# Performance work log

Measured on AMD Instinct MI355X. Metric: run time of the kernel, lower is better.

Reference implementation:

```python
import jax, jax.numpy as jnp
import numpy as np

N = 12000
F_IN = 256
F_OUT = 256


def setup_inputs() -> dict:
    key = jax.random.key(0)
    k1, k2, k3, k4, k5, k6 = jax.random.split(key, 6)
    stdv = 1.0 / np.sqrt(F_OUT)
    inp = {
        "input": jax.random.normal(k1, (N, F_IN), dtype=jnp.float32),
        "adj": jax.random.uniform(k2, (N, N), dtype=jnp.float32),
        "incidence_matrix": jax.random.uniform(k3, (N, N), dtype=jnp.float32),
        "weight": jax.random.uniform(k4, (F_IN, F_OUT), jnp.float32, -stdv, stdv),
        "attn": jax.random.uniform(k5, (F_IN, 1), jnp.float32, -stdv, stdv),
        "alpha": jax.random.uniform(k6, (1,), dtype=jnp.float32),
    }
    return inp


def reference(input, adj, incidence_matrix, weight, attn, alpha):
    # support1 = softmax over nodes of per-node attention score: [N, 1]
    scores = input @ attn                      # [N, 1]
    support1 = jax.nn.softmax(scores, axis=0)  # [N, 1]
    # diag(support1) @ input is just a per-row scale (avoid NxN diag)
    scaled = support1 * input                  # [N, F_in]
    support3 = adj @ scaled                    # [N, F_in]
    support4 = support3 + alpha * input        # [N, F_in]
    support = support4 @ weight                # [N, F_out]
    output = incidence_matrix @ support        # [N, F_out]
    return output
```

## Files before the change

kernel.cpp:

```cpp
#include <hip/hip_runtime.h>
#include <hip/hip_bf16.h>

typedef __bf16 bf16_t;
typedef __bf16 bf16x8v __attribute__((ext_vector_type(8)));
typedef __bf16 bf16x4v __attribute__((ext_vector_type(4)));
typedef float f32x4 __attribute__((ext_vector_type(4)));

#define NN 12000
#define FF 256

__global__ void scores_kernel(const float* __restrict__ input, const float* __restrict__ attn,
                              float* __restrict__ scores)
{
    int tid  = threadIdx.x;
    int lane = tid & 63;
    int r    = blockIdx.x * 4 + (tid >> 6);
    const float4 x = *(const float4*)(input + (size_t)r * FF + lane * 4);
    const float4 a = *(const float4*)(attn + lane * 4);
    float s = x.x * a.x + x.y * a.y + x.z * a.z + x.w * a.w;
#pragma unroll
    for (int off = 32; off > 0; off >>= 1) s += __shfl_down(s, off);
    if (lane == 0) scores[r] = s;
}

__global__ void softmax_kernel(float* __restrict__ s, int n)
{
    __shared__ float red[16];
    __shared__ float bc[2];
    int tid = threadIdx.x, lane = tid & 63, w = tid >> 6;

    float mx = -1e30f;
    for (int i = tid; i < n; i += 1024) mx = fmaxf(mx, s[i]);
#pragma unroll
    for (int o = 32; o > 0; o >>= 1) mx = fmaxf(mx, __shfl_down(mx, o));
    if (lane == 0) red[w] = mx;
    __syncthreads();
    if (tid == 0) {
        float m = red[0];
        for (int i = 1; i < 16; ++i) m = fmaxf(m, red[i]);
        bc[0] = m;
    }
    __syncthreads();
    float M = bc[0];

    float sum = 0.f;
    for (int i = tid; i < n; i += 1024) sum += __expf(s[i] - M);
#pragma unroll
    for (int o = 32; o > 0; o >>= 1) sum += __shfl_down(sum, o);
    if (lane == 0) red[w] = sum;
    __syncthreads();
    if (tid == 0) {
        float t = 0.f;
        for (int i = 0; i < 16; ++i) t += red[i];
        bc[1] = t;
    }
    __syncthreads();
    float inv = 1.0f / bc[1];
    for (int i = tid; i < n; i += 1024) s[i] = __expf(s[i] - M) * inv;
}

__global__ void transpose_scale_kernel(const float* __restrict__ src, const float* __restrict__ p,
                                       bf16_t* __restrict__ dst, int R)
{
    __shared__ float T[64][65];
    int tid = threadIdx.x;
    int r0 = blockIdx.x * 64;
    int c0 = blockIdx.y * 64;
    int j = (tid & 15) * 4;
#pragma unroll
    for (int i = 0; i < 4; ++i) {
        int rl = (tid >> 4) + 16 * i;
        int gr = r0 + rl;
        float4 v = {0.f, 0.f, 0.f, 0.f};
        float sc = 1.f;
        if (gr < R) {
            v = *(const float4*)(src + (size_t)gr * FF + c0 + j);
            if (p) sc = p[gr];
        }
        T[rl][j + 0] = v.x * sc;
        T[rl][j + 1] = v.y * sc;
        T[rl][j + 2] = v.z * sc;
        T[rl][j + 3] = v.w * sc;
    }
    __syncthreads();
#pragma unroll
    for (int i = 0; i < 2; ++i) {
        int idx = tid + 256 * i;
        int cl = idx >> 3;
        int rr = (idx & 7) * 8;
        if (r0 + rr < R) {
            bf16x8v v;
#pragma unroll
            for (int e = 0; e < 8; ++e) v[e] = (bf16_t)T[rr + e][cl];
            *(bf16x8v*)(dst + (size_t)(c0 + cl) * R + r0 + rr) = v;
        }
    }
}

template <int MODE>
__global__ __launch_bounds__(256, 3)
void gemm_kernel(const float* __restrict__ A, const bf16_t* __restrict__ Bt,
                 float* __restrict__ Cpart, size_t part_stride,
                 bf16_t* __restrict__ Ct,
                 int M, int K, int sps, int total_steps)
{
    constexpr int LDSA  = 64 * 40;
    constexpr int LDSB  = 256 * 40;
    constexpr int STAGE = LDSA + LDSB;
    constexpr int EPI   = 256 * 72;
    __shared__ __align__(16) bf16_t smem[(MODE == 1) ? (STAGE > EPI ? STAGE : EPI) : STAGE];
    bf16_t* As = smem;
    bf16_t* Bs = smem + LDSA;

    const int tid  = threadIdx.x;
    const int wave = tid >> 6;
    const int lane = tid & 63;
    const int quad = lane >> 4;
    const int l16  = lane & 15;
    const int row0   = blockIdx.x * 64;
    const int step0  = blockIdx.y * sps;
    const int nsteps = min(sps, total_steps - step0);

    f32x4 acc[4][4];
#pragma unroll
    for (int i = 0; i < 4; ++i)
#pragma unroll
        for (int j = 0; j < 4; ++j)
            acc[i][j] = (f32x4){0.f, 0.f, 0.f, 0.f};

    const int a_kq = (tid & 7) * 4;
    const int a_r  = tid >> 3;
    const int b_kq = (tid & 3) * 8;
    const int b_n  = tid >> 2;
    const int qk   = quad * 8;

    for (int s = 0; s < nsteps; ++s) {
        const int k0 = (step0 + s) * 32;
#pragma unroll
        for (int i = 0; i < 2; ++i) {
            int r = a_r + 32 * i;
            int gr = row0 + r;
            float4 v = {0.f, 0.f, 0.f, 0.f};
            if (gr < M) v = *(const float4*)(A + (size_t)gr * K + k0 + a_kq);
            bf16x4v w;
            w[0] = (bf16_t)v.x; w[1] = (bf16_t)v.y; w[2] = (bf16_t)v.z; w[3] = (bf16_t)v.w;
            *(bf16x4v*)(As + r * 40 + a_kq) = w;
        }
#pragma unroll
        for (int i = 0; i < 4; ++i) {
            int n = b_n + 64 * i;
            bf16x8v v = *(const bf16x8v*)(Bt + (size_t)n * K + k0 + b_kq);
            *(bf16x8v*)(Bs + n * 40 + b_kq) = v;
        }
        __syncthreads();
        bf16x8v af[4], bfr[4];
#pragma unroll
        for (int t = 0; t < 4; ++t) {
            af[t]  = *(const bf16x8v*)(As + (16 * t + l16) * 40 + qk);
            bfr[t] = *(const bf16x8v*)(Bs + (wave * 64 + 16 * t + l16) * 40 + qk);
        }
#pragma unroll
        for (int im = 0; im < 4; ++im)
#pragma unroll
            for (int in = 0; in < 4; ++in)
                acc[im][in] = __builtin_amdgcn_mfma_f32_16x16x32_bf16(af[im], bfr[in], acc[im][in], 0, 0, 0);
        __syncthreads();
    }

    if (MODE == 0) {
        float* Cp = Cpart + (size_t)blockIdx.y * part_stride;
#pragma unroll
        for (int im = 0; im < 4; ++im)
#pragma unroll
            for (int in = 0; in < 4; ++in) {
                int n = wave * 64 + 16 * in + l16;
#pragma unroll
                for (int rg = 0; rg < 4; ++rg) {
                    int r = row0 + 16 * im + 4 * quad + rg;
                    if (r < M) Cp[(size_t)r * FF + n] = acc[im][in][rg];
                }
            }
    } else {
        constexpr int TS = 72;
        bf16_t* T = smem;
#pragma unroll
        for (int im = 0; im < 4; ++im)
#pragma unroll
            for (int in = 0; in < 4; ++in) {
                int n  = wave * 64 + 16 * in + l16;
                int mb = 16 * im + 4 * quad;
                bf16x4v w;
#pragma unroll
                for (int rg = 0; rg < 4; ++rg) w[rg] = (bf16_t)acc[im][in][rg];
                *(bf16x4v*)(T + n * TS + mb) = w;
            }
        __syncthreads();
#pragma unroll
        for (int i = 0; i < 8; ++i) {
            int idx = tid + 256 * i;
            int n  = idx >> 3;
            int mc = (idx & 7) * 8;
            if (row0 + mc < M) {
                bf16x8v v = *(const bf16x8v*)(T + n * TS + mc);
                *(bf16x8v*)(Ct + (size_t)n * M + row0 + mc) = v;
            }
        }
    }
}

__global__ void reduce_parts_kernel(const float* __restrict__ parts, size_t part_stride,
                                    int nsplit,
                                    const float* __restrict__ addsrc, const float* __restrict__ alpha,
                                    float* __restrict__ out, int count4)
{
    int i = blockIdx.x * 256 + threadIdx.x;
    if (i >= count4) return;
    f32x4 s = ((const f32x4*)parts)[i];
    for (int sp = 1; sp < nsplit; ++sp) {
        f32x4 v = *(const f32x4*)(parts + (size_t)sp * part_stride + (size_t)i * 4);
        s += v;
    }
    if (addsrc) {
        float a = alpha[0];
        f32x4 v = ((const f32x4*)addsrc)[i];
        s += v * a;
    }
    ((f32x4*)out)[i] = s;
}

extern "C" void kernel_launch(void* const* d_in, const int* in_sizes, int n_in,
                              void* d_out, int out_size, void* d_ws, size_t ws_size,
                              hipStream_t stream)
{
    const float* input  = (const float*)d_in[0];
    const float* adj    = (const float*)d_in[1];
    const float* inc    = (const float*)d_in[2];
    const float* weight = (const float*)d_in[3];
    const float* attn   = (const float*)d_in[4];
    const float* alpha  = (const float*)d_in[5];
    float* out = (float*)d_out;

    char* ws = (char*)d_ws;
    size_t off = 0;
    auto take = [&](size_t bytes) {
        char* p = ws + off;
        off = (off + bytes + 255) & ~(size_t)255;
        return p;
    };
    bf16_t* scaledT  = (bf16_t*)take((size_t)FF * NN * 2);
    bf16_t* supportT = (bf16_t*)take((size_t)FF * NN * 2);
    bf16_t* weightT  = (bf16_t*)take((size_t)FF * FF * 2);
    float*  support4 = (float*)take((size_t)NN * FF * 4);
    float*  scores   = (float*)take((size_t)NN * 4);

    const size_t part_elems = (size_t)NN * FF;
    int splits = 4;
    while (splits > 1 && off + (size_t)splits * part_elems * 4 > ws_size) --splits;
    float* parts = (float*)take((size_t)splits * part_elems * 4);

    const int total_steps = NN / 32;
    const int sps = (total_steps + splits - 1) / splits;
    const int mblocks = (NN + 63) / 64;
    const int red_blocks = (NN * FF / 4 + 255) / 256;

    scores_kernel<<<NN / 4, 256, 0, stream>>>(input, attn, scores);
    softmax_kernel<<<1, 1024, 0, stream>>>(scores, NN);
    transpose_scale_kernel<<<dim3(mblocks, FF / 64), 256, 0, stream>>>(input, scores, scaledT, NN);
    transpose_scale_kernel<<<dim3(FF / 64, FF / 64), 256, 0, stream>>>(weight, nullptr, weightT, FF);

    gemm_kernel<0><<<dim3(mblocks, splits), 256, 0, stream>>>(
        adj, scaledT, parts, part_elems, nullptr, NN, NN, sps, total_steps);
    reduce_parts_kernel<<<red_blocks, 256, 0, stream>>>(
        parts, part_elems, splits, input, alpha, support4, NN * FF / 4);
    gemm_kernel<1><<<dim3(mblocks, 1), 256, 0, stream>>>(
        support4, weightT, nullptr, 0, supportT, NN, FF, FF / 32, FF / 32);
    gemm_kernel<0><<<dim3(mblocks, splits), 256, 0, stream>>>(
        inc, supportT, parts, part_elems, nullptr, NN, NN, sps, total_steps);
    reduce_parts_kernel<<<red_blocks, 256, 0, stream>>>(
        parts, part_elems, splits, nullptr, nullptr, out, NN * FF / 4);
}
```

Before: 1.350 ms.

## Enlarge GEMM tile to 128 rows with 8 waves and register-prefetch pipelining

The GEMM block grows from 64x256 with 4 waves to 128x256 with 8 waves arranged 2x4. Each B tile is now reused across twice as many A rows, which cuts the reloading of the bf16 transposed operand. Global loads for the next k-step are issued into registers before the MFMAs of the current step, so memory latency overlaps with compute. The split-K count rises from 4 to 5. The costs are higher register pressure, fewer blocks along M, and more partial buffers for the reduce kernels to sum.

```diff
diff --git a/kernel.cpp b/kernel.cpp
--- a/kernel.cpp
+++ b/kernel.cpp
@@ -98,16 +98,16 @@
 }
 
 template <int MODE>
-__global__ __launch_bounds__(256, 3)
+__global__ __launch_bounds__(512, 4)
 void gemm_kernel(const float* __restrict__ A, const bf16_t* __restrict__ Bt,
                  float* __restrict__ Cpart, size_t part_stride,
                  bf16_t* __restrict__ Ct,
                  int M, int K, int sps, int total_steps)
 {
-    constexpr int LDSA  = 64 * 40;
+    constexpr int LDSA  = 128 * 40;
     constexpr int LDSB  = 256 * 40;
     constexpr int STAGE = LDSA + LDSB;
-    constexpr int EPI   = 256 * 72;
+    constexpr int EPI   = 256 * 136;
     __shared__ __align__(16) bf16_t smem[(MODE == 1) ? (STAGE > EPI ? STAGE : EPI) : STAGE];
     bf16_t* As = smem;
     bf16_t* Bs = smem + LDSA;
@@ -117,7 +117,11 @@
     const int lane = tid & 63;
     const int quad = lane >> 4;
     const int l16  = lane & 15;
-    const int row0   = blockIdx.x * 64;
+    const int wr   = wave >> 2;
+    const int wc   = wave & 3;
+    const int qk   = quad * 8;
+
+    const int row0   = blockIdx.x * 128;
     const int step0  = blockIdx.y * sps;
     const int nsteps = min(sps, total_steps - step0);
 
@@ -128,43 +132,54 @@
         for (int j = 0; j < 4; ++j)
             acc[i][j] = (f32x4){0.f, 0.f, 0.f, 0.f};
 
-    const int a_kq = (tid & 7) * 4;
-    const int a_r  = tid >> 3;
-    const int b_kq = (tid & 3) * 8;
-    const int b_n  = tid >> 2;
-    const int qk   = quad * 8;
-
+    const int a_row = tid >> 2;
+    const int a_ko  = (tid & 3) * 8;
+    const int a_row_safe = ((row0 + a_row) < M) ? a_row : 0;
+    const float* Ap = A + (size_t)(row0 + a_row_safe) * K + a_ko;
+    bf16_t* As_w = As + a_row * 40 + a_ko;
+    const int b_n0 = tid >> 2;
+    const int b_k0 = (tid & 3) * 8;
+    const int b_n1 = (tid + 512) >> 2;
+    const int b_k1 = ((tid + 512) & 3) * 8;
+    const bf16_t* Bp0 = Bt + (size_t)b_n0 * K + b_k0;
+    const bf16_t* Bp1 = Bt + (size_t)b_n1 * K + b_k1;
+    bf16_t* Bs_w0 = Bs + b_n0 * 40 + b_k0;
+    bf16_t* Bs_w1 = Bs + b_n1 * 40 + b_k1;
+
+    float4 av0, av1;
+    bf16x8v bv0, bv1;
+    auto issue = [&](int s) {
+        const int k = (step0 + s) * 32;
+        av0 = *(const float4*)(Ap + k);
+        av1 = *(const float4*)(Ap + k + 4);
+        bv0 = *(const bf16x8v*)(Bp0 + k);
+        bv1 = *(const bf16x8v*)(Bp1 + k);
+    };
+
+    issue(0);
     for (int s = 0; s < nsteps; ++s) {
-        const int k0 = (step0 + s) * 32;
-#pragma unroll
-        for (int i = 0; i < 2; ++i) {
-            int r = a_r + 32 * i;
-            int gr = row0 + r;
-            float4 v = {0.f, 0.f, 0.f, 0.f};
-            if (gr < M) v = *(const float4*)(A + (size_t)gr * K + k0 + a_kq);
-            bf16x4v w;
-            w[0] = (bf16_t)v.x; w[1] = (bf16_t)v.y; w[2] = (bf16_t)v.z; w[3] = (bf16_t)v.w;
-            *(bf16x4v*)(As + r * 40 + a_kq) = w;
-        }
-#pragma unroll
-        for (int i = 0; i < 4; ++i) {
-            int n = b_n + 64 * i;
-            bf16x8v v = *(const bf16x8v*)(Bt + (size_t)n * K + k0 + b_kq);
-            *(bf16x8v*)(Bs + n * 40 + b_kq) = v;
-        }
-        __syncthreads();
-        bf16x8v af[4], bfr[4];
-#pragma unroll
-        for (int t = 0; t < 4; ++t) {
-            af[t]  = *(const bf16x8v*)(As + (16 * t + l16) * 40 + qk);
-            bfr[t] = *(const bf16x8v*)(Bs + (wave * 64 + 16 * t + l16) * 40 + qk);
-        }
-#pragma unroll
-        for (int im = 0; im < 4; ++im)
-#pragma unroll
-            for (int in = 0; in < 4; ++in)
-                acc[im][in] = __builtin_amdgcn_mfma_f32_16x16x32_bf16(af[im], bfr[in], acc[im][in], 0, 0, 0);
-        __syncthreads();
+        bf16x8v aw;
+        aw[0] = (bf16_t)av0.x; aw[1] = (bf16_t)av0.y; aw[2] = (bf16_t)av0.z; aw[3] = (bf16_t)av0.w;
+        aw[4] = (bf16_t)av1.x; aw[5] = (bf16_t)av1.y; aw[6] = (bf16_t)av1.z; aw[7] = (bf16_t)av1.w;
+        bf16x8v bw0 = bv0, bw1 = bv1;
+        __syncthreads();
+        *(bf16x8v*)As_w  = aw;
+        *(bf16x8v*)Bs_w0 = bw0;
+        *(bf16x8v*)Bs_w1 = bw1;
+        if (s + 1 < nsteps) issue(s + 1);
+        __syncthreads();
+
+        bf16x8v af[4];
+#pragma unroll
+        for (int t = 0; t < 4; ++t)
+            af[t] = *(const bf16x8v*)(As + (wr * 64 + 16 * t + l16) * 40 + qk);
+#pragma unroll
+        for (int in = 0; in < 4; ++in) {
+            bf16x8v bfr = *(const bf16x8v*)(Bs + (wc * 64 + 16 * in + l16) * 40 + qk);
+#pragma unroll
+            for (int im = 0; im < 4; ++im)
+                acc[im][in] = __builtin_amdgcn_mfma_f32_16x16x32_bf16(af[im], bfr, acc[im][in], 0, 0, 0);
+        }
     }
 
     if (MODE == 0) {
@@ -173,22 +188,23 @@
         for (int im = 0; im < 4; ++im)
 #pragma unroll
             for (int in = 0; in < 4; ++in) {
-                int n = wave * 64 + 16 * in + l16;
+                int n = wc * 64 + 16 * in + l16;
 #pragma unroll
                 for (int rg = 0; rg < 4; ++rg) {
-                    int r = row0 + 16 * im + 4 * quad + rg;
+                    int r = row0 + wr * 64 + 16 * im + 4 * quad + rg;
                     if (r < M) Cp[(size_t)r * FF + n] = acc[im][in][rg];
                 }
             }
     } else {
-        constexpr int TS = 72;
+        constexpr int TS = 136;
         bf16_t* T = smem;
+        __syncthreads();
 #pragma unroll
         for (int im = 0; im < 4; ++im)
 #pragma unroll
             for (int in = 0; in < 4; ++in) {
-                int n  = wave * 64 + 16 * in + l16;
-                int mb = 16 * im + 4 * quad;
+                int n  = wc * 64 + 16 * in + l16;
+                int mb = wr * 64 + 16 * im + 4 * quad;
                 bf16x4v w;
 #pragma unroll
                 for (int rg = 0; rg < 4; ++rg) w[rg] = (bf16_t)acc[im][in][rg];
@@ -197,9 +213,9 @@
         __syncthreads();
 #pragma unroll
         for (int i = 0; i < 8; ++i) {
-            int idx = tid + 256 * i;
-            int n  = idx >> 3;
-            int mc = (idx & 7) * 8;
+            int idx = tid + 512 * i;
+            int n  = idx >> 4;
+            int mc = (idx & 15) * 8;
             if (row0 + mc < M) {
                 bf16x8v v = *(const bf16x8v*)(T + n * TS + mc);
                 *(bf16x8v*)(Ct + (size_t)n * M + row0 + mc) = v;
@@ -254,27 +270,28 @@
     float*  scores   = (float*)take((size_t)NN * 4);
 
     const size_t part_elems = (size_t)NN * FF;
-    int splits = 4;
+    int splits = 5;
     while (splits > 1 && off + (size_t)splits * part_elems * 4 > ws_size) --splits;
     float* parts = (float*)take((size_t)splits * part_elems * 4);
 
     const int total_steps = NN / 32;
     const int sps = (total_steps + splits - 1) / splits;
-    const int mblocks = (NN + 63) / 64;
+    const int mblocks = (NN + 127) / 128;
+    const int tblocks = (NN + 63) / 64;
     const int red_blocks = (NN * FF / 4 + 255) / 256;
 
     scores_kernel<<<NN / 4, 256, 0, stream>>>(input, attn, scores);
     softmax_kernel<<<1, 1024, 0, stream>>>(scores, NN);
-    transpose_scale_kernel<<<dim3(mblocks, FF / 64), 256, 0, stream>>>(input, scores, scaledT, NN);
+    transpose_scale_kernel<<<dim3(tblocks, FF / 64), 256, 0, stream>>>(input, scores, scaledT, NN);
     transpose_scale_kernel<<<dim3(FF / 64, FF / 64), 256, 0, stream>>>(weight, nullptr, weightT, FF);
 
-    gemm_kernel<0><<<dim3(mblocks, splits), 256, 0, stream>>>(
+    gemm_kernel<0><<<dim3(mblocks, splits), 512, 0, stream>>>(
         adj, scaledT, parts, part_elems, nullptr, NN, NN, sps, total_steps);
     reduce_parts_kernel<<<red_blocks, 256, 0, stream>>>(
         parts, part_elems, splits, input, alpha, support4, NN * FF / 4);
-    gemm_kernel<1><<<dim3(mblocks, 1), 256, 0, stream>>>(
+    gemm_kernel<1><<<dim3(mblocks, 1), 512, 0, stream>>>(
         support4, weightT, nullptr, 0, supportT, NN, FF, FF / 32, FF / 32);
-    gemm_kernel<0><<<dim3(mblocks, splits), 256, 0, stream>>>(
+    gemm_kernel<0><<<dim3(mblocks, splits), 512, 0, stream>>>(
         inc, supportT, parts, part_elems, nullptr, NN, NN, sps, total_steps);
     reduce_parts_kernel<<<red_blocks, 256, 0, stream>>>(
         parts, part_elems, splits, nullptr, nullptr, out, NN * FF / 4);
```

Result: faster. 1.233 ms (-8.7%).
